# Performance work log

Hardware: AMD Instinct MI355X
Metric: run time of the kernel (lower is better)

The kernel has to match this reference:

```python
import jax, jax.numpy as jnp
import numpy as np

PS = 3          # patch_size
ALPHA = 0.5     # alpha_0 (no step() calls -> stays at init value)
A_CUBIC = -0.75 # torch bicubic kernel coefficient


def _cubic_w(t):
    at = jnp.abs(t)
    w1 = ((A_CUBIC + 2.0) * at - (A_CUBIC + 3.0)) * at * at + 1.0
    w2 = A_CUBIC * (((at - 5.0) * at + 8.0) * at - 4.0)
    return jnp.where(at <= 1.0, w1, jnp.where(at < 2.0, w2, 0.0))


def _resize_axis(x, out_size, axis):
    # bicubic, align_corners=True, border-clamped (matches torch.nn.functional.interpolate)
    in_size = x.shape[axis]
    scale = (in_size - 1) / (out_size - 1)
    coords = jnp.arange(out_size, dtype=x.dtype) * jnp.asarray(scale, x.dtype)
    i0 = jnp.floor(coords)
    frac = coords - i0
    offs = jnp.arange(-1, 3)
    idx = jnp.clip(i0.astype(jnp.int32)[:, None] + offs[None, :], 0, in_size - 1)
    w = _cubic_w(frac[:, None] - offs[None, :].astype(x.dtype))  # [out,4]
    xm = jnp.moveaxis(x, axis, -1)
    vals = xm[..., idx]                      # [..., out, 4]
    out = jnp.einsum('...ot,ot->...o', vals, w)
    return jnp.moveaxis(out, -1, axis)


def _bicubic(x, out_h, out_w):
    return _resize_axis(_resize_axis(x, out_h, 2), out_w, 3)


def _unfold(x, ps=PS):
    # [B,C,H,W] -> [B, (H/ps)*(W/ps), C, ps, ps], row-major over (H-chunk, W-chunk)
    B, C, H, W = x.shape
    x = x.reshape(B, C, H // ps, ps, W // ps, ps)
    x = x.transpose(0, 2, 4, 1, 3, 5)
    return x.reshape(B, -1, C, ps, ps)


def _fold(p, C, H, W, ps=PS):
    B = p.shape[0]
    x = p.reshape(B, H // ps, W // ps, C, ps, ps)
    x = x.transpose(0, 3, 1, 4, 2, 5)
    return x.reshape(B, C, H, W)


def _g_database(tar, ps=PS):
    B, C, H, W = tar.shape
    scales = [tar, _bicubic(tar, H // 2, W // 2), _bicubic(tar, H // 4, W // 4)]
    patches = []
    for i in range(1, ps):
        for j in range(1, ps):
            for s in scales:
                h, w = s.shape[2], s.shape[3]
                if ps < min(h, w):
                    patches.append(_unfold(s[:, :, i:h - (ps - i), j:w - (ps - j)], ps))
    for s in scales:
        patches.append(_unfold(s, ps))
    return jnp.concatenate(patches, axis=1)  # [B, G, C, ps, ps]


def setup_inputs() -> dict:
    key = jax.random.key(0)
    k1, k2 = jax.random.split(key)
    inp = jax.random.uniform(k1, (2, 3, 144, 144), dtype=jnp.float32)
    tar = jax.random.uniform(k2, (2, 3, 144, 144), dtype=jnp.float32)
    return {"inp": inp, "tar": tar}


def reference(inp, tar):
    B, C, H, W = tar.shape
    ps = PS
    D = C * ps * ps
    ipf = _unfold(inp, ps).reshape(B, -1, D)   # [B,N,D]
    tpf = _unfold(tar, ps).reshape(B, -1, D)
    gf = _g_database(tar, ps).reshape(B, -1, D)  # [B,G,D]

    # nearest-candidate selection is done under no_grad in the original
    gf_s = jax.lax.stop_gradient(gf)
    tpf_s = jax.lax.stop_gradient(tpf)
    ipf_s = jax.lax.stop_gradient(ipf)
    gn = jnp.sum(gf_s * gf_s, axis=-1)  # [B,G]

    def sqdist(a):  # sum of squared diffs over D: [B,G,N]
        an = jnp.sum(a * a, axis=-1)
        return an[:, None, :] + gn[:, :, None] - 2.0 * jnp.einsum('bnd,bgd->bgn', a, gf_s)

    l = ALPHA * sqdist(tpf_s) + (1.0 - ALPHA) * sqdist(ipf_s)  # [B,G,N]
    index = jnp.argmin(l, axis=1)                              # [B,N]
    sel = jnp.take_along_axis(gf_s, index[..., None], axis=1)  # [B,N,D]

    loss_p = jnp.abs(ipf - sel)  # L1Loss(reduction='none')
    loss_img = _fold(loss_p.reshape(B, -1, C, ps, ps), C, H, W, ps)
    sel_img = _fold(sel.reshape(B, -1, C, ps, ps), C, H, W, ps)
    return loss_img.mean(), sel_img
```

## Files before the change

### kernel.cpp

```cpp
#include <hip/hip_runtime.h>
#include <math.h>

#define A_CUBIC (-0.75f)
#define NB 2
#define NC 3
#define HH 144
#define NPB 2304
#define GG 14460
#define DD 27
#define DP 28
#define GSPLIT 112
#define GTILE 130

typedef float v2f __attribute__((ext_vector_type(2)));

__constant__ int c_seg_start[15] = {0,2209,2738,2859,5068,5597,5718,7927,8456,8577,10786,11315,11436,13740,14316};
__constant__ int c_seg_gw[15]    = {47,23,11, 47,23,11, 47,23,11, 47,23,11, 48,24,12};
__constant__ int c_seg_oy[15]    = {1,1,1, 1,1,1, 2,2,2, 2,2,2, 0,0,0};
__constant__ int c_seg_ox[15]    = {1,1,1, 2,2,2, 1,1,1, 2,2,2, 0,0,0};
__constant__ int c_seg_src[15]   = {0,1,2, 0,1,2, 0,1,2, 0,1,2, 0,1,2};

__device__ __forceinline__ float cubicw(float t) {
    float at = fabsf(t);
    if (at <= 1.0f) return ((A_CUBIC + 2.0f) * at - (A_CUBIC + 3.0f)) * at * at + 1.0f;
    if (at < 2.0f)  return A_CUBIC * (((at - 5.0f) * at + 8.0f) * at - 4.0f);
    return 0.0f;
}

__global__ void prep_k(const float* __restrict__ tar, const float* __restrict__ inp,
                       float* __restrict__ s1, float* __restrict__ s2,
                       float* __restrict__ m, unsigned long long* __restrict__ best) {
    int t = blockIdx.x * 256 + threadIdx.x;
    const int total1 = NB * NC * 72 * 72;
    const int total2 = NB * NC * 36 * 36;
    if (t < total1 + total2) {
        float* dst; int O; int idx;
        if (t < total1) { dst = s1; O = 72; idx = t; }
        else            { dst = s2; O = 36; idx = t - total1; }
        int x  = idx % O;
        int y  = (idx / O) % O;
        int bc = idx / (O * O);
        const float* src = tar + (size_t)bc * HH * HH;
        float scale = (float)(143.0 / (double)(O - 1));
        float fy = (float)y * scale;
        float iyf = floorf(fy); float fry = fy - iyf; int iy = (int)iyf;
        float fx = (float)x * scale;
        float ixf = floorf(fx); float frx = fx - ixf; int ix = (int)ixf;
        float wy[4], wx[4];
        #pragma unroll
        for (int d = 0; d < 4; ++d) {
            wy[d] = cubicw(fry - (float)(d - 1));
            wx[d] = cubicw(frx - (float)(d - 1));
        }
        float acc = 0.0f;
        #pragma unroll
        for (int dx = 0; dx < 4; ++dx) {
            int cx = min(max(ix - 1 + dx, 0), HH - 1);
            float inner = 0.0f;
            #pragma unroll
            for (int dy = 0; dy < 4; ++dy) {
                int cy = min(max(iy - 1 + dy, 0), HH - 1);
                inner += wy[dy] * src[cy * HH + cx];
            }
            acc += wx[dx] * inner;
        }
        dst[idx] = acc;
    } else {
        int u = t - (total1 + total2);
        if (u >= NB * NPB) return;
        int b = u / NPB, n = u % NPB;
        int hc = n / 48, wc = n % 48;
        const float* ib = inp + (size_t)b * NC * HH * HH;
        const float* tb = tar + (size_t)b * NC * HH * HH;
        float* row = m + (size_t)u * DP;
        #pragma unroll
        for (int c = 0; c < 3; ++c)
            #pragma unroll
            for (int dy = 0; dy < 3; ++dy)
                #pragma unroll
                for (int dx = 0; dx < 3; ++dx) {
                    int off = (c * HH + hc * 3 + dy) * HH + wc * 3 + dx;
                    row[(c * 3 + dy) * 3 + dx] = ib[off] + tb[off];
                }
        row[27] = -1.0f;
        best[u] = 0ULL;
    }
}

__global__ void build_gf_k(const float* __restrict__ tar, const float* __restrict__ s1,
                           const float* __restrict__ s2, float* __restrict__ gf) {
    int t = blockIdx.x * 256 + threadIdx.x;
    if (t >= NB * GG) return;
    int b = t / GG, g = t % GG;
    int s = 0;
    #pragma unroll
    for (int k = 1; k < 15; ++k) if (g >= c_seg_start[k]) s = k;
    int p  = g - c_seg_start[s];
    int gw = c_seg_gw[s];
    int hc = p / gw, wc = p % gw;
    int oy = c_seg_oy[s], ox = c_seg_ox[s];
    int srci = c_seg_src[s];
    const float* img; int sz;
    if (srci == 0)      { img = tar; sz = 144; }
    else if (srci == 1) { img = s1;  sz = 72;  }
    else                { img = s2;  sz = 36;  }
    const float* base = img + (size_t)b * NC * sz * sz;
    int y0 = oy + hc * 3, x0 = ox + wc * 3;
    float acc = 0.0f;
    float* row = gf + (size_t)t * DP;
    #pragma unroll
    for (int c = 0; c < 3; ++c)
        #pragma unroll
        for (int dy = 0; dy < 3; ++dy)
            #pragma unroll
            for (int dx = 0; dx < 3; ++dx) {
                float v = base[((size_t)c * sz + y0 + dy) * sz + x0 + dx];
                row[(c * 3 + dy) * 3 + dx] = v;
                acc = fmaf(v, v, acc);
            }
    row[27] = acc;
}

__device__ __forceinline__ float dot28(const v2f mr[14], const v2f r[14]) {
    v2f a0 = {0.0f, 0.0f}, a1 = {0.0f, 0.0f};
    #pragma unroll
    for (int i = 0; i < 14; i += 2) {
        a0 = __builtin_elementwise_fma(mr[i],     r[i],     a0);
        a1 = __builtin_elementwise_fma(mr[i + 1], r[i + 1], a1);
    }
    v2f t = a0 + a1;
    return t.x + t.y;
}

__global__ __launch_bounds__(256, 8) void argmin_k(
        const float* __restrict__ gf, const float* __restrict__ m,
        unsigned long long* __restrict__ best) {
    int tid = threadIdx.x;
    int nblk = blockIdx.y;
    int b  = nblk / 9;
    int nn = nblk * 256 + tid;
    const v2f* mrow = (const v2f*)(m + (size_t)nn * DP);
    v2f mr[14];
    #pragma unroll
    for (int i = 0; i < 14; ++i) mr[i] = mrow[i];
    int g0 = blockIdx.x * GTILE;
    int g1 = min(g0 + GTILE, GG);
    const float* gfb = gf + (size_t)b * GG * DP;
    float bv = -3.0e38f; int bi = 0;

    v2f A[14], B[14];
    {
        const v2f* p = (const v2f*)(gfb + (size_t)g0 * DP);
        #pragma unroll
        for (int i = 0; i < 14; ++i) A[i] = p[i];
    }
    int g = g0;
    for (; g + 1 < g1; g += 2) {
        {
            const v2f* p = (const v2f*)(gfb + (size_t)(g + 1) * DP);
            #pragma unroll
            for (int i = 0; i < 14; ++i) B[i] = p[i];
        }
        float s = dot28(mr, A);
        if (s > bv) { bv = s; bi = g; }
        {
            const v2f* p = (const v2f*)(gfb + (size_t)(g + 2) * DP);
            #pragma unroll
            for (int i = 0; i < 14; ++i) A[i] = p[i];
        }
        float s2 = dot28(mr, B);
        if (s2 > bv) { bv = s2; bi = g + 1; }
    }
    if (g < g1) {
        float s = dot28(mr, A);
        if (s > bv) { bv = s; bi = g; }
    }
    unsigned u = __float_as_uint(bv);
    u ^= (unsigned)(((int)u >> 31)) | 0x80000000u;
    unsigned long long packed = ((unsigned long long)u << 32) | (unsigned)(~bi);
    atomicMax(&best[nn], packed);
}

__global__ void finalize_k(const float* __restrict__ gf,
                           const unsigned long long* __restrict__ best,
                           const float* __restrict__ inp,
                           float* __restrict__ out, float* __restrict__ lpart) {
    __shared__ float red[256];
    int t = blockIdx.x * 256 + threadIdx.x;
    float lsum = 0.0f;
    if (t < NB * NPB) {
        int b = t / NPB, n = t % NPB;
        unsigned long long pk = best[t];
        int bi = (int)(~(unsigned)(pk & 0xFFFFFFFFull));
        int hc = n / 48, wc = n % 48;
        const float* grow = gf + ((size_t)b * GG + bi) * DP;
        const float* ib   = inp + (size_t)b * NC * HH * HH;
        float* sel = out + 1 + (size_t)b * NC * HH * HH;
        #pragma unroll
        for (int c = 0; c < 3; ++c)
            #pragma unroll
            for (int dy = 0; dy < 3; ++dy)
                #pragma unroll
                for (int dx = 0; dx < 3; ++dx) {
                    int d = (c * 3 + dy) * 3 + dx;
                    float sv = grow[d];
                    int off = (c * HH + hc * 3 + dy) * HH + wc * 3 + dx;
                    sel[off] = sv;
                    lsum += fabsf(ib[off] - sv);
                }
    }
    red[threadIdx.x] = lsum;
    __syncthreads();
    for (int s = 128; s > 0; s >>= 1) {
        if (threadIdx.x < s) red[threadIdx.x] += red[threadIdx.x + s];
        __syncthreads();
    }
    if (threadIdx.x == 0) lpart[blockIdx.x] = red[0];
}

__global__ void sum_k(const float* __restrict__ lpart, float* __restrict__ out) {
    if (threadIdx.x == 0) {
        float s = 0.0f;
        for (int i = 0; i < 18; ++i) s += lpart[i];
        out[0] = s * (1.0f / 124416.0f);
    }
}

extern "C" void kernel_launch(void* const* d_in, const int* in_sizes, int n_in,
                              void* d_out, int out_size, void* d_ws, size_t ws_size,
                              hipStream_t stream) {
    const float* inp = (const float*)d_in[0];
    const float* tar = (const float*)d_in[1];
    float* out = (float*)d_out;
    float* ws  = (float*)d_ws;

    float* s1 = ws;
    float* s2 = s1 + 31104;
    float* gf = s2 + 7776;
    float* m  = gf + 809760;
    unsigned long long* best = (unsigned long long*)(m + 129024);
    float* lp = (float*)(best + 4608);

    prep_k    <<<(43488 + 255) / 256, 256, 0, stream>>>(tar, inp, s1, s2, m, best);
    build_gf_k<<<(28920 + 255) / 256, 256, 0, stream>>>(tar, s1, s2, gf);
    argmin_k  <<<dim3(GSPLIT, 18), 256, 0, stream>>>(gf, m, best);
    finalize_k<<<18, 256, 0, stream>>>(gf, best, inp, out, lp);
    sum_k     <<<1, 64, 0, stream>>>(lp, out);
}
```

Before: 68.66 us.

## Register-block argmin kernel over three query patches per thread

Each thread in the argmin kernel now holds three query rows (n, n+256, n+512) in registers. Every candidate row loaded from gf is reused across three dot products, which cuts global/L2 load traffic per FMA by about three times. The grid shrinks from 18 to 6 query blocks, so the G split goes up to 128 tiles of 113 to keep enough blocks. Launch bounds drop occupancy to 4 waves per SIMD to make room for the extra registers, which costs latency hiding.

Result: faster. 66.49 us (-3.2%).

```diff
diff --git a/kernel.cpp b/kernel.cpp
--- a/kernel.cpp
+++ b/kernel.cpp
@@ -9,8 +9,8 @@
 #define GG 14460
 #define DD 27
 #define DP 28
-#define GSPLIT 112
-#define GTILE 130
+#define GSPLIT 128
+#define GTILE 113
 
 typedef float v2f __attribute__((ext_vector_type(2)));
 
@@ -121,32 +121,36 @@
     row[27] = acc;
 }
 
-__device__ __forceinline__ float dot28(const v2f mr[14], const v2f r[14]) {
-    v2f a0 = {0.0f, 0.0f}, a1 = {0.0f, 0.0f};
-    #pragma unroll
-    for (int i = 0; i < 14; i += 2) {
-        a0 = __builtin_elementwise_fma(mr[i],     r[i],     a0);
-        a1 = __builtin_elementwise_fma(mr[i + 1], r[i + 1], a1);
-    }
-    v2f t = a0 + a1;
-    return t.x + t.y;
-}
-
-__global__ __launch_bounds__(256, 8) void argmin_k(
+__device__ __forceinline__ void dot28x3(const v2f r0[14], const v2f r1[14], const v2f r2[14],
+                                        const v2f gR[14], float& s0, float& s1, float& s2) {
+    v2f a0 = {0.0f, 0.0f}, a1 = {0.0f, 0.0f}, a2 = {0.0f, 0.0f};
+    #pragma unroll
+    for (int i = 0; i < 14; ++i) {
+        a0 = __builtin_elementwise_fma(r0[i], gR[i], a0);
+        a1 = __builtin_elementwise_fma(r1[i], gR[i], a1);
+        a2 = __builtin_elementwise_fma(r2[i], gR[i], a2);
+    }
+    s0 = a0.x + a0.y; s1 = a1.x + a1.y; s2 = a2.x + a2.y;
+}
+
+__global__ __launch_bounds__(256, 4) void argmin_k(
         const float* __restrict__ gf, const float* __restrict__ m,
         unsigned long long* __restrict__ best) {
     int tid = threadIdx.x;
-    int nblk = blockIdx.y;
-    int b  = nblk / 9;
-    int nn = nblk * 256 + tid;
-    const v2f* mrow = (const v2f*)(m + (size_t)nn * DP);
-    v2f mr[14];
-    #pragma unroll
-    for (int i = 0; i < 14; ++i) mr[i] = mrow[i];
+    int nb = blockIdx.y;
+    int b  = nb / 3;
+    int n0 = nb * 768 + tid;
+    const v2f* m0 = (const v2f*)(m + (size_t)n0 * DP);
+    const v2f* m1 = (const v2f*)(m + (size_t)(n0 + 256) * DP);
+    const v2f* m2 = (const v2f*)(m + (size_t)(n0 + 512) * DP);
+    v2f r0[14], r1[14], r2[14];
+    #pragma unroll
+    for (int i = 0; i < 14; ++i) { r0[i] = m0[i]; r1[i] = m1[i]; r2[i] = m2[i]; }
     int g0 = blockIdx.x * GTILE;
     int g1 = min(g0 + GTILE, GG);
     const float* gfb = gf + (size_t)b * GG * DP;
-    float bv = -3.0e38f; int bi = 0;
+    float bv0 = -3.0e38f, bv1 = -3.0e38f, bv2 = -3.0e38f;
+    int   bi0 = 0,        bi1 = 0,        bi2 = 0;
 
     v2f A[14], B[14];
     {
@@ -161,24 +165,34 @@
             #pragma unroll
             for (int i = 0; i < 14; ++i) B[i] = p[i];
         }
-        float s = dot28(mr, A);
-        if (s > bv) { bv = s; bi = g; }
+        float s0, s1, s2;
+        dot28x3(r0, r1, r2, A, s0, s1, s2);
+        if (s0 > bv0) { bv0 = s0; bi0 = g; }
+        if (s1 > bv1) { bv1 = s1; bi1 = g; }
+        if (s2 > bv2) { bv2 = s2; bi2 = g; }
         {
             const v2f* p = (const v2f*)(gfb + (size_t)(g + 2) * DP);
             #pragma unroll
             for (int i = 0; i < 14; ++i) A[i] = p[i];
         }
-        float s2 = dot28(mr, B);
-        if (s2 > bv) { bv = s2; bi = g + 1; }
+        dot28x3(r0, r1, r2, B, s0, s1, s2);
+        if (s0 > bv0) { bv0 = s0; bi0 = g + 1; }
+        if (s1 > bv1) { bv1 = s1; bi1 = g + 1; }
+        if (s2 > bv2) { bv2 = s2; bi2 = g + 1; }
     }
     if (g < g1) {
-        float s = dot28(mr, A);
-        if (s > bv) { bv = s; bi = g; }
-    }
-    unsigned u = __float_as_uint(bv);
-    u ^= (unsigned)(((int)u >> 31)) | 0x80000000u;
-    unsigned long long packed = ((unsigned long long)u << 32) | (unsigned)(~bi);
-    atomicMax(&best[nn], packed);
+        float s0, s1, s2;
+        dot28x3(r0, r1, r2, A, s0, s1, s2);
+        if (s0 > bv0) { bv0 = s0; bi0 = g; }
+        if (s1 > bv1) { bv1 = s1; bi1 = g; }
+        if (s2 > bv2) { bv2 = s2; bi2 = g; }
+    }
+    unsigned u0 = __float_as_uint(bv0); u0 ^= (unsigned)(((int)u0 >> 31)) | 0x80000000u;
+    unsigned u1 = __float_as_uint(bv1); u1 ^= (unsigned)(((int)u1 >> 31)) | 0x80000000u;
+    unsigned u2 = __float_as_uint(bv2); u2 ^= (unsigned)(((int)u2 >> 31)) | 0x80000000u;
+    atomicMax(&best[n0],       ((unsigned long long)u0 << 32) | (unsigned)(~bi0));
+    atomicMax(&best[n0 + 256], ((unsigned long long)u1 << 32) | (unsigned)(~bi1));
+    atomicMax(&best[n0 + 512], ((unsigned long long)u2 << 32) | (unsigned)(~bi2));
 }
 
 __global__ void finalize_k(const float* __restrict__ gf,
@@ -243,7 +257,7 @@
 
     prep_k    <<<(43488 + 255) / 256, 256, 0, stream>>>(tar, inp, s1, s2, m, best);
     build_gf_k<<<(28920 + 255) / 256, 256, 0, stream>>>(tar, s1, s2, gf);
-    argmin_k  <<<dim3(GSPLIT, 18), 256, 0, stream>>>(gf, m, best);
+    argmin_k  <<<dim3(GSPLIT, 6), 256, 0, stream>>>(gf, m, best);
     finalize_k<<<18, 256, 0, stream>>>(gf, best, inp, out, lp);
     sum_k     <<<1, 64, 0, stream>>>(lp, out);
 }
```
